# Optimization experiments

Hardware: AMD Instinct MI355X
Metric: run time of the kernel (lower is better)

## Reference

```python
import jax, jax.numpy as jnp
import numpy as np

N = 100000          # nodes
E = 3200000         # edges (avg degree 32)
D_IN = 64           # node_in
D_OUT = 64          # out_channels (heads=1)
NEG_SLOPE = 0.2     # PyG GATConv default
EPS = 1e-5          # BatchNorm eps


def setup_inputs() -> dict:
    key = jax.random.key(0)
    ks = jax.random.split(key, 6)
    node_feats = jax.random.normal(ks[0], (N, D_IN), dtype=jnp.float32)
    edge_index = jax.random.randint(ks[1], (2, E), 0, N, dtype=jnp.int64)
    W = jax.random.normal(ks[2], (D_IN, D_OUT), dtype=jnp.float32) / np.sqrt(D_IN)
    att_src = jax.random.normal(ks[3], (D_OUT,), dtype=jnp.float32) * 0.1
    att_dst = jax.random.normal(ks[4], (D_OUT,), dtype=jnp.float32) * 0.1
    bias = jnp.zeros((D_OUT,), dtype=jnp.float32)
    gamma = jnp.ones((D_OUT,), dtype=jnp.float32)
    beta = jnp.zeros((D_OUT,), dtype=jnp.float32)
    return {"node_feats": node_feats, "edge_index": edge_index, "W": W,
            "att_src": att_src, "att_dst": att_dst, "bias": bias,
            "gamma": gamma, "beta": beta}


def reference(node_feats, edge_index, W, att_src, att_dst, bias, gamma, beta):
    n = node_feats.shape[0]
    # Linear transform: (N, D_OUT)
    x = node_feats @ W
    # Add self-loops (PyG GATConv default add_self_loops=True)
    loops = jnp.arange(n, dtype=edge_index.dtype)
    src = jnp.concatenate([edge_index[0], loops])  # (E+N,)
    dst = jnp.concatenate([edge_index[1], loops])
    # Per-node attention logits, gathered per edge
    a_src = x @ att_src  # (N,)
    a_dst = x @ att_dst  # (N,)
    e = jax.nn.leaky_relu(a_src[src] + a_dst[dst], NEG_SLOPE)  # (E+N,)
    # Scatter-softmax over incoming edges of each destination node
    m = jax.ops.segment_max(e, dst, num_segments=n)
    ex = jnp.exp(e - m[dst])
    s = jax.ops.segment_sum(ex, dst, num_segments=n)
    alpha = ex / s[dst]  # (E+N,)
    # Weighted scatter-add aggregation of transformed source features
    out = jax.ops.segment_sum(x[src] * alpha[:, None], dst, num_segments=n) + bias
    # BatchNorm1d (training-mode batch statistics) + ReLU
    mu = out.mean(axis=0)
    var = out.var(axis=0)
    out = (out - mu) / jnp.sqrt(var + EPS) * gamma + beta
    return jax.nn.relu(out)
```

## Files before the change

kernel.cpp:

```cpp
#include <hip/hip_runtime.h>
#include <hip/hip_fp16.h>

#define NN 100000
#define NE 3200000
#define NEG_SLOPE 0.2f
#define BN_EPS 1e-5f
#define NBUK 196
#define CAP 17400
#define CHUNK 4096
#define NB_A 782

__device__ __forceinline__ unsigned short f2bf(float f) {
    unsigned u = __float_as_uint(f);
    return (unsigned short)((u + 0x7FFFu + ((u >> 16) & 1u)) >> 16);
}
__device__ __forceinline__ float bf2f(unsigned short h) {
    return __uint_as_float((unsigned)h << 16);
}
__device__ __forceinline__ float wdec(unsigned u) {
    return __half2float(__ushort_as_half((unsigned short)(u >> 17)));
}
__device__ __forceinline__ int detect64(const int* __restrict__ idx) {
    int any = 0;
#pragma unroll
    for (int k = 0; k < 16; ++k) any |= idx[2 * k + 1];
    return any == 0;
}

__global__ __launch_bounds__(256) void transform_kernel(
    const float* __restrict__ feats, const float* __restrict__ W,
    const float* __restrict__ att_s, const float* __restrict__ att_d,
    unsigned short* __restrict__ xb, float* __restrict__ a_src, float* __restrict__ a_dst) {
    int n = blockIdx.x * 256 + threadIdx.x;
    if (n >= NN) return;
    float acc[64];
#pragma unroll
    for (int j = 0; j < 64; ++j) acc[j] = 0.f;
    const float4* fr = (const float4*)(feats + (size_t)n * 64);
    for (int q = 0; q < 16; ++q) {
        float4 f = fr[q];
#pragma unroll
        for (int j = 0; j < 64; ++j) acc[j] = fmaf(f.x, W[(4 * q + 0) * 64 + j], acc[j]);
#pragma unroll
        for (int j = 0; j < 64; ++j) acc[j] = fmaf(f.y, W[(4 * q + 1) * 64 + j], acc[j]);
#pragma unroll
        for (int j = 0; j < 64; ++j) acc[j] = fmaf(f.z, W[(4 * q + 2) * 64 + j], acc[j]);
#pragma unroll
        for (int j = 0; j < 64; ++j) acc[j] = fmaf(f.w, W[(4 * q + 3) * 64 + j], acc[j]);
    }
    float as = 0.f, ad = 0.f;
#pragma unroll
    for (int j = 0; j < 64; ++j) {
        as = fmaf(acc[j], att_s[j], as);
        ad = fmaf(acc[j], att_d[j], ad);
    }
    unsigned w32[32];
#pragma unroll
    for (int j = 0; j < 32; ++j)
        w32[j] = (unsigned)f2bf(acc[2 * j]) | ((unsigned)f2bf(acc[2 * j + 1]) << 16);
    uint4* xr = (uint4*)(xb + (size_t)n * 64);
#pragma unroll
    for (int q = 0; q < 8; ++q)
        xr[q] = make_uint4(w32[4 * q], w32[4 * q + 1], w32[4 * q + 2], w32[4 * q + 3]);
    a_src[n] = as;
    a_dst[n] = ad;
}

__global__ __launch_bounds__(256) void binA_kernel(const int* __restrict__ idx,
                                                   int* __restrict__ gcur,
                                                   unsigned* __restrict__ pairs) {
    __shared__ int hist[256];
    __shared__ int gbase[256];
    int t = threadIdx.x;
    int is64 = detect64(idx);
    int c0 = blockIdx.x * CHUNK;
    int cnt = min(CHUNK, NE - c0);
    hist[t] = 0;
    __syncthreads();
    unsigned pk[16];
    int bks[16], rks[16];
#pragma unroll
    for (int k = 0; k < 16; ++k) {
        int j = t + k * 256;
        rks[k] = -1;
        if (j < cnt) {
            int i = c0 + j;
            int sn, dn;
            if (is64) { sn = ((const int2*)idx)[i].x; dn = ((const int2*)idx)[(size_t)NE + i].x; }
            else      { sn = idx[i];                  dn = idx[NE + i]; }
            int b = dn >> 9;
            bks[k] = b;
            pk[k] = ((unsigned)(dn & 511) << 17) | (unsigned)sn;
            rks[k] = atomicAdd(&hist[b], 1);
        }
    }
    __syncthreads();
    if (hist[t]) gbase[t] = atomicAdd(&gcur[t], hist[t]);
    __syncthreads();
#pragma unroll
    for (int k = 0; k < 16; ++k)
        if (rks[k] >= 0) {
            int rel = gbase[bks[k]] + rks[k];
            if (rel < CAP) pairs[(size_t)bks[k] * CAP + rel] = pk[k];
        }
}

__global__ __launch_bounds__(512) void sortB_kernel(const unsigned* __restrict__ pairs,
                                                    const int* __restrict__ gcur,
                                                    const float* __restrict__ a_src,
                                                    const float* __restrict__ a_dst,
                                                    int* __restrict__ row_ptr,
                                                    int* __restrict__ row_end,
                                                    unsigned* __restrict__ csr) {
    __shared__ int hist[512];
    __shared__ int curs[512];
    __shared__ float ads[512];
    int b = blockIdx.x;
    int t = threadIdx.x;
    int base = b * CAP;
    int end = base + min(gcur[b], CAP);
    hist[t] = 0;
    int node = (b << 9) + t;
    ads[t] = (node < NN) ? a_dst[node] : 0.f;
    __syncthreads();
    for (int i = base + t; i < end; i += 512)
        atomicAdd(&hist[pairs[i] >> 17], 1);
    __syncthreads();
    int v = hist[t];
    for (int off = 1; off < 512; off <<= 1) {
        int add = (t >= off) ? hist[t - off] : 0;
        __syncthreads();
        hist[t] += add;
        __syncthreads();
    }
    int lofs = hist[t] - v;
    curs[t] = lofs;
    if (node < NN) {
        row_ptr[node] = base + lofs;
        row_end[node] = base + lofs + v;
    }
    __syncthreads();
    for (int i = base + t; i < end; i += 512) {
        unsigned u = pairs[i];
        int dl = u >> 17;
        int sn = (int)(u & 0x1FFFF);
        float e = a_src[sn] + ads[dl];
        e = fmaxf(e, NEG_SLOPE * e);
        float w = __expf(e);
        unsigned short hb = __half_as_ushort(__float2half(w));
        int pos = atomicAdd(&curs[dl], 1);
        csr[base + pos] = ((unsigned)hb << 17) | (unsigned)sn;
    }
}

__global__ __launch_bounds__(256) void aggregate_csr_kernel(
    const int* __restrict__ row_ptr, const int* __restrict__ row_end,
    const unsigned* __restrict__ csr, const unsigned short* __restrict__ xb,
    const float* __restrict__ a_src, const float* __restrict__ a_dst,
    float* __restrict__ out, float* __restrict__ stats) {
    int lane = threadIdx.x & 63;
    int w = threadIdx.x >> 6;
    int wid = blockIdx.x * 4 + w;
    int nw = gridDim.x * 4;
    float bn0 = 0.f, bn1 = 0.f;
    for (int n = wid; n < NN; n += nw) {
        int row0 = __builtin_amdgcn_readfirstlane(row_ptr[n]);
        int row1 = __builtin_amdgcn_readfirstlane(row_end[n]);
        float ad = a_dst[n];
        float es = a_src[n] + ad;
        es = fmaxf(es, NEG_SLOPE * es);
        float wself = __expf(es);
        float acc = wself * bf2f(xb[((size_t)n << 6) + lane]);
        float ssum = wself;
        for (int e = row0; e < row1; e += 16) {
            unsigned u[16];
#pragma unroll
            for (int j = 0; j < 16; ++j) u[j] = csr[e + j];
            float v[16];
#pragma unroll
            for (int j = 0; j < 16; ++j)
                v[j] = bf2f(xb[((size_t)(u[j] & 0x1FFFFu) << 6) + lane]);
#pragma unroll
            for (int j = 0; j < 16; ++j) {
                float wv = (e + j < row1) ? wdec(u[j]) : 0.f;
                acc = fmaf(wv, v[j], acc);
                ssum += wv;
            }
        }
        float o = acc * __builtin_amdgcn_rcpf(ssum);
        out[((size_t)n << 6) + lane] = o;
        bn0 += o;
        bn1 = fmaf(o, o, bn1);
    }
    __shared__ float l0[4][64], l1[4][64];
    l0[w][lane] = bn0;
    l1[w][lane] = bn1;
    __syncthreads();
    if (threadIdx.x < 64) {
        float t0 = l0[0][lane] + l0[1][lane] + l0[2][lane] + l0[3][lane];
        float t1 = l1[0][lane] + l1[1][lane] + l1[2][lane] + l1[3][lane];
        unsafeAtomicAdd(&stats[lane], t0);
        unsafeAtomicAdd(&stats[64 + lane], t1);
    }
}

__global__ __launch_bounds__(256) void bn_norm_kernel(float* __restrict__ out,
                                                      const float* __restrict__ stats,
                                                      const float* __restrict__ gamma,
                                                      const float* __restrict__ beta) {
    __shared__ float sc[64], sh[64];
    int t = threadIdx.x;
    if (t < 64) {
        float mu = stats[t] * (1.0f / NN);
        float var = stats[64 + t] * (1.0f / NN) - mu * mu;
        float s = gamma[t] * rsqrtf(var + BN_EPS);
        sc[t] = s;
        sh[t] = fmaf(-mu, s, beta[t]);
    }
    __syncthreads();
    int stride = gridDim.x * 256;
    int total = NN * 16;
    for (int i = blockIdx.x * 256 + t; i < total; i += stride) {
        float4 v = ((const float4*)out)[i];
        int c = (i & 15) * 4;
        v.x = fmaxf(0.f, fmaf(v.x, sc[c + 0], sh[c + 0]));
        v.y = fmaxf(0.f, fmaf(v.y, sc[c + 1], sh[c + 1]));
        v.z = fmaxf(0.f, fmaf(v.z, sc[c + 2], sh[c + 2]));
        v.w = fmaxf(0.f, fmaf(v.w, sc[c + 3], sh[c + 3]));
        ((float4*)out)[i] = v;
    }
}

extern "C" void kernel_launch(void* const* d_in, const int* in_sizes, int n_in,
                              void* d_out, int out_size, void* d_ws, size_t ws_size,
                              hipStream_t stream) {
    const float* feats = (const float*)d_in[0];
    const int* idx     = (const int*)d_in[1];
    const float* W     = (const float*)d_in[2];
    const float* att_s = (const float*)d_in[3];
    const float* att_d = (const float*)d_in[4];
    const float* gamma = (const float*)d_in[6];
    const float* beta  = (const float*)d_in[7];
    float* out = (float*)d_out;

    unsigned short* xb = (unsigned short*)d_ws;
    float* a_src    = (float*)d_ws + (size_t)NN * 32;
    float* a_dst    = a_src + NN;
    int* gcur       = (int*)(a_dst + NN);
    float* stats    = (float*)(gcur + 256);
    int* row_ptr    = (int*)(stats + 128);
    int* row_end    = row_ptr + NN;
    unsigned* pairs = (unsigned*)(row_end + NN);
    unsigned* csr   = pairs + (size_t)NBUK * CAP;

    hipMemsetAsync(gcur, 0, (256 + 128) * sizeof(int), stream);

    transform_kernel<<<(NN + 255) / 256, 256, 0, stream>>>(feats, W, att_s, att_d, xb, a_src, a_dst);
    binA_kernel<<<NB_A, 256, 0, stream>>>(idx, gcur, pairs);
    sortB_kernel<<<NBUK, 512, 0, stream>>>(pairs, gcur, a_src, a_dst, row_ptr, row_end, csr);
    aggregate_csr_kernel<<<2048, 256, 0, stream>>>(row_ptr, row_end, csr, xb, a_src, a_dst, out, stats);
    bn_norm_kernel<<<2048, 256, 0, stream>>>(out, stats, gamma, beta);
}
```

Before: 311.1 us.

## Split wavefront into four edge groups with 8-byte feature gathers

Restructures the CSR aggregation so each wavefront handles four edges at once. Each 16-lane quarter gathers a full 64-channel bf16 row as uint2 (4 channels per lane) instead of every lane loading one 2-byte element per edge. Partial sums are combined with cross-lane xor shuffles, and only one quarter writes the output and BN statistics. The aim is wider, fewer memory transactions per gathered row. In exchange it adds shuffle reductions and runs fewer edges in flight per loop iteration (4 per step, 16 total as before).

```diff
diff --git a/kernel.cpp b/kernel.cpp
--- a/kernel.cpp
+++ b/kernel.cpp
@@ -17,6 +17,8 @@
 __device__ __forceinline__ float bf2f(unsigned short h) {
     return __uint_as_float((unsigned)h << 16);
 }
+__device__ __forceinline__ float blo(unsigned v) { return __uint_as_float(v << 16); }
+__device__ __forceinline__ float bhi(unsigned v) { return __uint_as_float(v & 0xFFFF0000u); }
 __device__ __forceinline__ float wdec(unsigned u) {
     return __half2float(__ushort_as_half((unsigned short)(u >> 17)));
 }
@@ -160,9 +162,11 @@
     float* __restrict__ out, float* __restrict__ stats) {
     int lane = threadIdx.x & 63;
     int w = threadIdx.x >> 6;
+    int q = lane >> 4;
+    int c16 = lane & 15;
     int wid = blockIdx.x * 4 + w;
     int nw = gridDim.x * 4;
-    float bn0 = 0.f, bn1 = 0.f;
+    float bn0[4] = {0.f, 0.f, 0.f, 0.f}, bn1[4] = {0.f, 0.f, 0.f, 0.f};
     for (int n = wid; n < NN; n += nw) {
         int row0 = __builtin_amdgcn_readfirstlane(row_ptr[n]);
         int row1 = __builtin_amdgcn_readfirstlane(row_end[n]);
@@ -170,37 +174,54 @@
         float es = a_src[n] + ad;
         es = fmaxf(es, NEG_SLOPE * es);
         float wself = __expf(es);
-        float acc = wself * bf2f(xb[((size_t)n << 6) + lane]);
-        float ssum = wself;
+        float wq = (q == 0) ? wself : 0.f;
+        uint2 ds = ((const uint2*)(xb + ((size_t)n << 6)))[c16];
+        float a0 = wq * blo(ds.x), a1 = wq * bhi(ds.x);
+        float a2 = wq * blo(ds.y), a3 = wq * bhi(ds.y);
+        float ssum = wq;
         for (int e = row0; e < row1; e += 16) {
-            unsigned u[16];
-#pragma unroll
-            for (int j = 0; j < 16; ++j) u[j] = csr[e + j];
-            float v[16];
-#pragma unroll
-            for (int j = 0; j < 16; ++j)
-                v[j] = bf2f(xb[((size_t)(u[j] & 0x1FFFFu) << 6) + lane]);
-#pragma unroll
-            for (int j = 0; j < 16; ++j) {
-                float wv = (e + j < row1) ? wdec(u[j]) : 0.f;
-                acc = fmaf(wv, v[j], acc);
+#pragma unroll
+            for (int s = 0; s < 4; ++s) {
+                int ei = e + 4 * s + q;
+                unsigned um = csr[ei];
+                uint2 d = ((const uint2*)(xb + ((size_t)(um & 0x1FFFFu) << 6)))[c16];
+                float wv = (ei < row1) ? wdec(um) : 0.f;
+                a0 = fmaf(wv, blo(d.x), a0);
+                a1 = fmaf(wv, bhi(d.x), a1);
+                a2 = fmaf(wv, blo(d.y), a2);
+                a3 = fmaf(wv, bhi(d.y), a3);
                 ssum += wv;
             }
         }
-        float o = acc * __builtin_amdgcn_rcpf(ssum);
-        out[((size_t)n << 6) + lane] = o;
-        bn0 += o;
-        bn1 = fmaf(o, o, bn1);
+        a0 += __shfl_xor(a0, 16, 64); a0 += __shfl_xor(a0, 32, 64);
+        a1 += __shfl_xor(a1, 16, 64); a1 += __shfl_xor(a1, 32, 64);
+        a2 += __shfl_xor(a2, 16, 64); a2 += __shfl_xor(a2, 32, 64);
+        a3 += __shfl_xor(a3, 16, 64); a3 += __shfl_xor(a3, 32, 64);
+        ssum += __shfl_xor(ssum, 16, 64); ssum += __shfl_xor(ssum, 32, 64);
+        float inv = __builtin_amdgcn_rcpf(ssum);
+        float o0 = a0 * inv, o1 = a1 * inv, o2 = a2 * inv, o3 = a3 * inv;
+        if (q == 0) {
+            ((float4*)(out + ((size_t)n << 6)))[c16] = make_float4(o0, o1, o2, o3);
+            bn0[0] += o0; bn1[0] = fmaf(o0, o0, bn1[0]);
+            bn0[1] += o1; bn1[1] = fmaf(o1, o1, bn1[1]);
+            bn0[2] += o2; bn1[2] = fmaf(o2, o2, bn1[2]);
+            bn0[3] += o3; bn1[3] = fmaf(o3, o3, bn1[3]);
+        }
     }
     __shared__ float l0[4][64], l1[4][64];
-    l0[w][lane] = bn0;
-    l1[w][lane] = bn1;
+    if (q == 0) {
+#pragma unroll
+        for (int k = 0; k < 4; ++k) {
+            l0[w][c16 * 4 + k] = bn0[k];
+            l1[w][c16 * 4 + k] = bn1[k];
+        }
+    }
     __syncthreads();
     if (threadIdx.x < 64) {
-        float t0 = l0[0][lane] + l0[1][lane] + l0[2][lane] + l0[3][lane];
-        float t1 = l1[0][lane] + l1[1][lane] + l1[2][lane] + l1[3][lane];
-        unsafeAtomicAdd(&stats[lane], t0);
-        unsafeAtomicAdd(&stats[64 + lane], t1);
+        float t0 = l0[0][threadIdx.x] + l0[1][threadIdx.x] + l0[2][threadIdx.x] + l0[3][threadIdx.x];
+        float t1 = l1[0][threadIdx.x] + l1[1][threadIdx.x] + l1[2][threadIdx.x] + l1[3][threadIdx.x];
+        unsafeAtomicAdd(&stats[threadIdx.x], t0);
+        unsafeAtomicAdd(&stats[64 + threadIdx.x], t1);
     }
 }
 
```

New measurement: 315.0 us. About the same (+1.3%).
